# Kernel tuning notes

Hardware: AMD Instinct MI355X
Metric: run time of the kernel (lower is better)

The kernel has to match this reference:

```python
import jax, jax.numpy as jnp
import numpy as np

N_NODES = 100000
N_EDGES = 1600000
F_IN = 128
HIDDEN = 64
N_CLASSES = 32


def setup_inputs() -> dict:
    key = jax.random.key(0)
    k1, k2, k3, k4 = jax.random.split(key, 4)
    x = jax.random.normal(k1, (N_NODES, F_IN), dtype=jnp.float32)
    edge_index = jax.random.randint(k2, (2, N_EDGES), 0, N_NODES, dtype=jnp.int32)
    # Glorot-style init for the two GCNConv weight matrices
    W1 = jax.random.normal(k3, (F_IN, HIDDEN), dtype=jnp.float32) * (1.0 / np.sqrt(F_IN))
    W2 = jax.random.normal(k4, (HIDDEN, N_CLASSES), dtype=jnp.float32) * (1.0 / np.sqrt(HIDDEN))
    b1 = jnp.zeros((HIDDEN,), dtype=jnp.float32)
    b2 = jnp.zeros((N_CLASSES,), dtype=jnp.float32)
    return {"x": x, "edge_index": edge_index, "W1": W1, "b1": b1, "W2": W2, "b2": b2}


def gcn_conv(x, W, b, src, dst, num_nodes):
    # PyG GCNConv: linear transform first, then normalized neighbor aggregation.
    h = x @ W  # [N, out]
    ones = jnp.ones(src.shape, dtype=h.dtype)
    deg = jax.ops.segment_sum(ones, dst, num_segments=num_nodes)  # in-degree incl. self-loops
    d_inv_sqrt = jnp.where(deg > 0, jax.lax.rsqrt(deg), 0.0)
    norm = d_inv_sqrt[src] * d_inv_sqrt[dst]  # [E]
    msg = h[src] * norm[:, None]              # gather + scale, [E, out]
    out = jax.ops.segment_sum(msg, dst, num_segments=num_nodes)  # scatter-add
    return out + b


def reference(x, edge_index, W1, b1, W2, b2):
    n = x.shape[0]
    # add_self_loops=True (GCNConv default)
    loop = jnp.arange(n, dtype=edge_index.dtype)
    src = jnp.concatenate([edge_index[0], loop])
    dst = jnp.concatenate([edge_index[1], loop])
    h = jax.nn.relu(gcn_conv(x, W1, b1, src, dst, n))
    # F.dropout(training=self.training) is identity in eval mode
    logits = gcn_conv(h, W2, b2, src, dst, n)
    return jax.nn.log_softmax(logits, axis=1)
```

## Files before the change

### kernel.cpp

```cpp
#include <hip/hip_runtime.h>

#define F_IN 128
#define HID 64
#define CLS 32
#define BCAP 8192

typedef short v8s __attribute__((ext_vector_type(8)));
typedef float f4 __attribute__((ext_vector_type(4)));
typedef float f2 __attribute__((ext_vector_type(2)));

__device__ __forceinline__ float bflo(unsigned int w) { return __uint_as_float(w << 16); }
__device__ __forceinline__ float bfhi(unsigned int w) { return __uint_as_float(w & 0xFFFF0000u); }
__device__ __forceinline__ unsigned short f2bf(float f) {
    unsigned int u = __float_as_uint(f);
    u += 0x7FFFu + ((u >> 16) & 1u);
    return (unsigned short)(u >> 16);
}
__device__ __forceinline__ unsigned int pack2(float lo, float hi) {
    return (unsigned int)f2bf(lo) | ((unsigned int)f2bf(hi) << 16);
}
__device__ __forceinline__ unsigned int relu2(unsigned int w) {
    unsigned int lo = (w & 0x8000u) ? 0u : (w & 0xFFFFu);
    unsigned int hi = (w & 0x80000000u) ? 0u : (w & 0xFFFF0000u);
    return lo | hi;
}
__device__ __forceinline__ unsigned char f2fp8(float v) {
    return (unsigned char)(__builtin_amdgcn_cvt_pk_fp8_f32(v, v, 0, false) & 0xFF);
}

__global__ __launch_bounds__(512) void k_init(int* __restrict__ bCursor, int nb) {
    int i = threadIdx.x;
    if (i < nb) bCursor[i] = i * BCAP;
}

__global__ __launch_bounds__(256) void k_bscatter(const int* __restrict__ src,
                                                  const int* __restrict__ dst,
                                                  int* __restrict__ bCursor,
                                                  int* __restrict__ bucketed, int E, int nb) {
    __shared__ int h[512];
    __shared__ int chunk[512];
    int tid = threadIdx.x;
    for (int i = tid; i < nb; i += 256) h[i] = 0;
    __syncthreads();

    int e0 = blockIdx.x * 2048;
    int myRec[8], myB[8], myRank[8];
#pragma unroll
    for (int k = 0; k < 8; ++k) {
        int e = e0 + k * 256 + tid;
        if (e < E) {
            int d = dst[e];
            myB[k] = d >> 8;
            myRec[k] = src[e] | ((d & 255) << 17);
            myRank[k] = atomicAdd(&h[myB[k]], 1);
        } else {
            myB[k] = -1;
        }
    }
    __syncthreads();
    for (int i = tid; i < nb; i += 256)
        chunk[i] = h[i] ? atomicAdd(&bCursor[i], h[i]) : 0;
    __syncthreads();
#pragma unroll
    for (int k = 0; k < 8; ++k) {
        if (myB[k] >= 0) bucketed[chunk[myB[k]] + myRank[k]] = myRec[k];
    }
}

__global__ __launch_bounds__(256) void k_csr(const int* __restrict__ bCursor,
                                             const int* __restrict__ bucketed,
                                             int* __restrict__ offs, int* __restrict__ ends,
                                             float* __restrict__ dinv, int* __restrict__ csr,
                                             int n) {
    __shared__ int cnt[256];
    __shared__ int s[256];
    __shared__ int cur[256];
    int b = blockIdx.x;
    int node0 = b << 8;
    int tid = threadIdx.x;
    int node = node0 + tid;
    cnt[tid] = 0;
    __syncthreads();
    int p0 = b * BCAP, p1 = bCursor[b];
    for (int p = p0 + tid; p < p1; p += 256) {
        int rec = bucketed[p];
        atomicAdd(&cnt[rec >> 17], 1);
    }
    __syncthreads();
    int v = cnt[tid];
    s[tid] = v;
    __syncthreads();
    for (int off = 1; off < 256; off <<= 1) {
        int t = (tid >= off) ? s[tid - off] : 0;
        __syncthreads();
        s[tid] += t;
        __syncthreads();
    }
    int myoff = p0 + s[tid] - v;
    cur[tid] = myoff;
    if (node < n) {
        offs[node] = myoff;
        ends[node] = myoff + v;
        dinv[node] = rsqrtf((float)(v + 1));
    }
    __syncthreads();
    for (int p = p0 + tid; p < p1; p += 256) {
        int rec = bucketed[p];
        int pos = atomicAdd(&cur[rec >> 17], 1);
        csr[pos] = rec & 0x1FFFF;
    }
}

__global__ __launch_bounds__(256) void k_gemm1(const float* __restrict__ x,
                                               const float* __restrict__ W,
                                               const float* __restrict__ dinv,
                                               unsigned char* __restrict__ y, int n) {
    __shared__ unsigned short Wt[HID * 136];
    int tid = threadIdx.x;
    for (int i = tid; i < F_IN * HID; i += 256) {
        int k = i >> 6, nn = i & 63;
        Wt[nn * 136 + k] = f2bf(W[i]);
    }
    __syncthreads();

    int lane = tid & 63;
    int quad = lane >> 4, c = lane & 15;
    int nstripes = (n + 31) >> 5;
    int stripe = blockIdx.x * 4 + (tid >> 6);
    if (stripe >= nstripes) return;
    int row0 = stripe << 5;

    f4 acc[2][4] = {};
    union { unsigned int u[4]; v8s v; } au;

#pragma unroll
    for (int ks = 0; ks < 4; ++ks) {
        int k0 = ks * 32 + quad * 8;
        v8s a[2];
#pragma unroll
        for (int mt = 0; mt < 2; ++mt) {
            int row = row0 + mt * 16 + c;
            if (row >= n) row = n - 1;
            const float* xp = x + (size_t)row * F_IN + k0;
            float4 lo = *(const float4*)xp;
            float4 hi = *(const float4*)(xp + 4);
            au.u[0] = pack2(lo.x, lo.y);
            au.u[1] = pack2(lo.z, lo.w);
            au.u[2] = pack2(hi.x, hi.y);
            au.u[3] = pack2(hi.z, hi.w);
            a[mt] = au.v;
        }
#pragma unroll
        for (int nt = 0; nt < 4; ++nt) {
            v8s b = *(const v8s*)&Wt[(nt * 16 + c) * 136 + k0];
            acc[0][nt] = __builtin_amdgcn_mfma_f32_16x16x32_bf16(a[0], b, acc[0][nt], 0, 0, 0);
            acc[1][nt] = __builtin_amdgcn_mfma_f32_16x16x32_bf16(a[1], b, acc[1][nt], 0, 0, 0);
        }
    }

#pragma unroll
    for (int mt = 0; mt < 2; ++mt)
#pragma unroll
        for (int reg = 0; reg < 4; ++reg) {
            int row = row0 + mt * 16 + quad * 4 + reg;
            if (row < n) {
                float dd = dinv[row];
#pragma unroll
                for (int nt = 0; nt < 4; ++nt)
                    y[(size_t)row * HID + nt * 16 + c] = f2fp8(acc[mt][nt][reg] * dd);
            }
        }
}

__global__ __launch_bounds__(256) void k_gemm2(const unsigned short* __restrict__ hb,
                                               const float* __restrict__ W,
                                               const float* __restrict__ dinv,
                                               unsigned short* __restrict__ y, int n) {
    __shared__ unsigned short Wt[CLS * 72];
    int tid = threadIdx.x;
    for (int i = tid; i < HID * CLS; i += 256) {
        int k = i >> 5, nn = i & 31;
        Wt[nn * 72 + k] = f2bf(W[i]);
    }
    __syncthreads();

    int lane = tid & 63;
    int quad = lane >> 4, c = lane & 15;
    int nstripes = (n + 31) >> 5;
    int stripe = blockIdx.x * 4 + (tid >> 6);
    if (stripe >= nstripes) return;
    int row0 = stripe << 5;

    f4 acc[2][2] = {};
    union { unsigned int u[4]; v8s v; } au;

#pragma unroll
    for (int ks = 0; ks < 2; ++ks) {
        int k0 = ks * 32 + quad * 8;
        v8s a[2];
#pragma unroll
        for (int mt = 0; mt < 2; ++mt) {
            int row = row0 + mt * 16 + c;
            if (row >= n) row = n - 1;
            uint4 w = *(const uint4*)(hb + (size_t)row * HID + k0);
            au.u[0] = relu2(w.x);
            au.u[1] = relu2(w.y);
            au.u[2] = relu2(w.z);
            au.u[3] = relu2(w.w);
            a[mt] = au.v;
        }
#pragma unroll
        for (int nt = 0; nt < 2; ++nt) {
            v8s b = *(const v8s*)&Wt[(nt * 16 + c) * 72 + k0];
            acc[0][nt] = __builtin_amdgcn_mfma_f32_16x16x32_bf16(a[0], b, acc[0][nt], 0, 0, 0);
            acc[1][nt] = __builtin_amdgcn_mfma_f32_16x16x32_bf16(a[1], b, acc[1][nt], 0, 0, 0);
        }
    }

#pragma unroll
    for (int mt = 0; mt < 2; ++mt)
#pragma unroll
        for (int reg = 0; reg < 4; ++reg) {
            int row = row0 + mt * 16 + quad * 4 + reg;
            if (row < n) {
                float dd = dinv[row];
#pragma unroll
                for (int nt = 0; nt < 2; ++nt)
                    y[(size_t)row * CLS + nt * 16 + c] = f2bf(acc[mt][nt][reg] * dd);
            }
        }
}

__global__ __launch_bounds__(256) void k_gather64(const int* __restrict__ offs,
                                                  const int* __restrict__ ends,
                                                  const int* __restrict__ csr,
                                                  const float* __restrict__ dinv,
                                                  const unsigned char* __restrict__ xw8,
                                                  const float* __restrict__ b,
                                                  unsigned short* __restrict__ hb, int n) {
    int node = blockIdx.x * 16 + (threadIdx.x >> 4);
    if (node >= n) return;
    int l = threadIdx.x & 15;
    int p0 = offs[node], p1 = ends[node];

    unsigned int sw = *(const unsigned int*)(xw8 + (size_t)node * HID + l * 4);
    float dd = dinv[node];

    f2 A0 = {0.f, 0.f}, A1 = A0, B0 = A0, B1 = A0, C0 = A0, C1 = A0, D0 = A0, D1 = A0;
    int p = p0;
    for (; p + 3 < p1; p += 4) {
        int s0 = csr[p], s1 = csr[p + 1], s2 = csr[p + 2], s3 = csr[p + 3];
        unsigned int w0 = *(const unsigned int*)(xw8 + (size_t)s0 * HID + l * 4);
        unsigned int w1 = *(const unsigned int*)(xw8 + (size_t)s1 * HID + l * 4);
        unsigned int w2 = *(const unsigned int*)(xw8 + (size_t)s2 * HID + l * 4);
        unsigned int w3 = *(const unsigned int*)(xw8 + (size_t)s3 * HID + l * 4);
        A0 += __builtin_amdgcn_cvt_pk_f32_fp8(w0, false);
        A1 += __builtin_amdgcn_cvt_pk_f32_fp8(w0, true);
        B0 += __builtin_amdgcn_cvt_pk_f32_fp8(w1, false);
        B1 += __builtin_amdgcn_cvt_pk_f32_fp8(w1, true);
        C0 += __builtin_amdgcn_cvt_pk_f32_fp8(w2, false);
        C1 += __builtin_amdgcn_cvt_pk_f32_fp8(w2, true);
        D0 += __builtin_amdgcn_cvt_pk_f32_fp8(w3, false);
        D1 += __builtin_amdgcn_cvt_pk_f32_fp8(w3, true);
    }
    for (; p < p1; ++p) {
        int s = csr[p];
        unsigned int w = *(const unsigned int*)(xw8 + (size_t)s * HID + l * 4);
        A0 += __builtin_amdgcn_cvt_pk_f32_fp8(w, false);
        A1 += __builtin_amdgcn_cvt_pk_f32_fp8(w, true);
    }
    A0 += B0; C0 += D0; A0 += C0;
    A1 += B1; C1 += D1; A1 += C1;

    A0 += __builtin_amdgcn_cvt_pk_f32_fp8(sw, false);
    A1 += __builtin_amdgcn_cvt_pk_f32_fp8(sw, true);
    float4 bb = *(const float4*)(b + l * 4);
    uint2 o;
    o.x = pack2(A0.x * dd + bb.x, A0.y * dd + bb.y);
    o.y = pack2(A1.x * dd + bb.z, A1.y * dd + bb.w);
    *(uint2*)(hb + (size_t)node * HID + l * 4) = o;
}

__global__ __launch_bounds__(256) void k_gather32_lsm(const int* __restrict__ offs,
                                                      const int* __restrict__ ends,
                                                      const int* __restrict__ csr,
                                                      const float* __restrict__ dinv,
                                                      const unsigned short* __restrict__ hwb,
                                                      const float* __restrict__ b,
                                                      float* __restrict__ out, int n) {
    int node = blockIdx.x * 16 + (threadIdx.x >> 4);
    if (node >= n) return;
    int l = threadIdx.x & 15;
    int p0 = offs[node], p1 = ends[node];

    unsigned int sw = *(const unsigned int*)(hwb + (size_t)node * CLS + l * 2);
    float dd = dinv[node];

    float A0 = 0.f, A1 = 0.f, B0 = 0.f, B1 = 0.f, C0 = 0.f, C1 = 0.f, D0 = 0.f, D1 = 0.f;
    int p = p0;
    for (; p + 3 < p1; p += 4) {
        int s0 = csr[p], s1 = csr[p + 1], s2 = csr[p + 2], s3 = csr[p + 3];
        unsigned int w0 = *(const unsigned int*)(hwb + (size_t)s0 * CLS + l * 2);
        unsigned int w1 = *(const unsigned int*)(hwb + (size_t)s1 * CLS + l * 2);
        unsigned int w2 = *(const unsigned int*)(hwb + (size_t)s2 * CLS + l * 2);
        unsigned int w3 = *(const unsigned int*)(hwb + (size_t)s3 * CLS + l * 2);
        A0 += bflo(w0); A1 += bfhi(w0);
        B0 += bflo(w1); B1 += bfhi(w1);
        C0 += bflo(w2); C1 += bfhi(w2);
        D0 += bflo(w3); D1 += bfhi(w3);
    }
    for (; p < p1; ++p) {
        int s = csr[p];
        unsigned int w = *(const unsigned int*)(hwb + (size_t)s * CLS + l * 2);
        A0 += bflo(w); A1 += bfhi(w);
    }
    A0 += B0; C0 += D0; A0 += C0;
    A1 += B1; C1 += D1; A1 += C1;

    float v0 = (A0 + bflo(sw)) * dd + b[l * 2];
    float v1 = (A1 + bfhi(sw)) * dd + b[l * 2 + 1];

    float m = fmaxf(v0, v1);
    m = fmaxf(m, __shfl_xor(m, 1));
    m = fmaxf(m, __shfl_xor(m, 2));
    m = fmaxf(m, __shfl_xor(m, 4));
    m = fmaxf(m, __shfl_xor(m, 8));
    float s = __expf(v0 - m) + __expf(v1 - m);
    s += __shfl_xor(s, 1);
    s += __shfl_xor(s, 2);
    s += __shfl_xor(s, 4);
    s += __shfl_xor(s, 8);
    float ls = m + __logf(s);
    float2 o;
    o.x = v0 - ls;
    o.y = v1 - ls;
    *(float2*)(out + (size_t)node * CLS + l * 2) = o;
}

extern "C" void kernel_launch(void* const* d_in, const int* in_sizes, int n_in,
                              void* d_out, int out_size, void* d_ws, size_t ws_size,
                              hipStream_t stream) {
    const float* x  = (const float*)d_in[0];
    const int* edge = (const int*)d_in[1];
    const float* W1 = (const float*)d_in[2];
    const float* b1 = (const float*)d_in[3];
    const float* W2 = (const float*)d_in[4];
    const float* b2 = (const float*)d_in[5];
    float* out = (float*)d_out;

    int N = in_sizes[0] / F_IN;
    int E = in_sizes[1] / 2;
    const int* src = edge;
    const int* dst = edge + E;
    int NB = (N + 255) >> 8;

    float* dinv    = (float*)d_ws;
    int* offs      = (int*)(dinv + N);
    int* ends      = offs + N;
    int* bCursor   = ends + N;
    int* csr       = bCursor + 512;
    int* bucketed  = csr + (size_t)NB * BCAP;
    unsigned char* bufA = (unsigned char*)(bucketed + (size_t)NB * BCAP);
    unsigned short* bufB = (unsigned short*)(bufA + (size_t)N * HID);

    k_init<<<1, 512, 0, stream>>>(bCursor, NB);
    k_bscatter<<<(E + 2047) / 2048, 256, 0, stream>>>(src, dst, bCursor, bucketed, E, NB);
    k_csr<<<NB, 256, 0, stream>>>(bCursor, bucketed, offs, ends, dinv, csr, N);

    int nstripes = (N + 31) >> 5;
    int gemmBlocks = (nstripes + 3) / 4;
    int gatherBlocks = (N + 15) / 16;

    k_gemm1<<<gemmBlocks, 256, 0, stream>>>(x, W1, dinv, bufA, N);
    k_gather64<<<gatherBlocks, 256, 0, stream>>>(offs, ends, csr, dinv, bufA, b1, bufB, N);

    k_gemm2<<<gemmBlocks, 256, 0, stream>>>(bufB, W2, dinv, (unsigned short*)bufA, N);
    k_gather32_lsm<<<gatherBlocks, 256, 0, stream>>>(offs, ends, csr, dinv, (unsigned short*)bufA, b2, out, N);
}
```

Before: 219.5 us.

## Sort nodes by degree per block, pack offset/count, unroll gather by 8

```diff
diff --git a/kernel.cpp b/kernel.cpp
--- a/kernel.cpp
+++ b/kernel.cpp
@@ -69,17 +69,20 @@
 
 __global__ __launch_bounds__(256) void k_csr(const int* __restrict__ bCursor,
                                              const int* __restrict__ bucketed,
-                                             int* __restrict__ offs, int* __restrict__ ends,
+                                             int* __restrict__ pk,
                                              float* __restrict__ dinv, int* __restrict__ csr,
-                                             int n) {
+                                             int* __restrict__ order, int n) {
     __shared__ int cnt[256];
     __shared__ int s[256];
     __shared__ int cur[256];
+    __shared__ int hist[64];
+    __shared__ int hbase[64];
     int b = blockIdx.x;
     int node0 = b << 8;
     int tid = threadIdx.x;
     int node = node0 + tid;
     cnt[tid] = 0;
+    if (tid < 64) hist[tid] = 0;
     __syncthreads();
     int p0 = b * BCAP, p1 = bCursor[b];
     for (int p = p0 + tid; p < p1; p += 256) {
@@ -89,6 +92,8 @@
     __syncthreads();
     int v = cnt[tid];
     s[tid] = v;
+    int dkey = (node < n) ? (v > 63 ? 63 : v) : 0;
+    atomicAdd(&hist[dkey], 1);
     __syncthreads();
     for (int off = 1; off < 256; off <<= 1) {
         int t = (tid >= off) ? s[tid - off] : 0;
@@ -96,18 +101,23 @@
         s[tid] += t;
         __syncthreads();
     }
+    if (tid == 0) {
+        int acc = 0;
+        for (int d = 63; d >= 0; --d) { hbase[d] = acc; acc += hist[d]; }
+    }
     int myoff = p0 + s[tid] - v;
     cur[tid] = myoff;
     if (node < n) {
-        offs[node] = myoff;
-        ends[node] = myoff + v;
+        pk[node] = myoff | (v << 22);
         dinv[node] = rsqrtf((float)(v + 1));
     }
     __syncthreads();
+    int pos = atomicAdd(&hbase[dkey], 1);
+    order[node0 + pos] = node;
     for (int p = p0 + tid; p < p1; p += 256) {
         int rec = bucketed[p];
-        int pos = atomicAdd(&cur[rec >> 17], 1);
-        csr[pos] = rec & 0x1FFFF;
+        int q = atomicAdd(&cur[rec >> 17], 1);
+        csr[q] = rec & 0x1FFFF;
     }
 }
 
@@ -231,29 +241,35 @@
         }
 }
 
-__global__ __launch_bounds__(256) void k_gather64(const int* __restrict__ offs,
-                                                  const int* __restrict__ ends,
+__global__ __launch_bounds__(256) void k_gather64(const int* __restrict__ order,
+                                                  const int* __restrict__ pk,
                                                   const int* __restrict__ csr,
-                                                  const float* __restrict__ dinv,
                                                   const unsigned char* __restrict__ xw8,
                                                   const float* __restrict__ b,
                                                   unsigned short* __restrict__ hb, int n) {
-    int node = blockIdx.x * 16 + (threadIdx.x >> 4);
+    int node = order[blockIdx.x * 16 + (threadIdx.x >> 4)];
     if (node >= n) return;
     int l = threadIdx.x & 15;
-    int p0 = offs[node], p1 = ends[node];
-
+    unsigned int pv = (unsigned int)pk[node];
+    int p0 = pv & 0x3FFFFF;
+    int cntv = pv >> 22;
+    int p1 = p0 + cntv;
+    float dd = rsqrtf((float)(cntv + 1));
     unsigned int sw = *(const unsigned int*)(xw8 + (size_t)node * HID + l * 4);
-    float dd = dinv[node];
 
     f2 A0 = {0.f, 0.f}, A1 = A0, B0 = A0, B1 = A0, C0 = A0, C1 = A0, D0 = A0, D1 = A0;
     int p = p0;
-    for (; p + 3 < p1; p += 4) {
-        int s0 = csr[p], s1 = csr[p + 1], s2 = csr[p + 2], s3 = csr[p + 3];
+    for (; p + 7 < p1; p += 8) {
+        int s0 = csr[p],     s1 = csr[p + 1], s2 = csr[p + 2], s3 = csr[p + 3];
+        int s4 = csr[p + 4], s5 = csr[p + 5], s6 = csr[p + 6], s7 = csr[p + 7];
         unsigned int w0 = *(const unsigned int*)(xw8 + (size_t)s0 * HID + l * 4);
         unsigned int w1 = *(const unsigned int*)(xw8 + (size_t)s1 * HID + l * 4);
         unsigned int w2 = *(const unsigned int*)(xw8 + (size_t)s2 * HID + l * 4);
         unsigned int w3 = *(const unsigned int*)(xw8 + (size_t)s3 * HID + l * 4);
+        unsigned int w4 = *(const unsigned int*)(xw8 + (size_t)s4 * HID + l * 4);
+        unsigned int w5 = *(const unsigned int*)(xw8 + (size_t)s5 * HID + l * 4);
+        unsigned int w6 = *(const unsigned int*)(xw8 + (size_t)s6 * HID + l * 4);
+        unsigned int w7 = *(const unsigned int*)(xw8 + (size_t)s7 * HID + l * 4);
         A0 += __builtin_amdgcn_cvt_pk_f32_fp8(w0, false);
         A1 += __builtin_amdgcn_cvt_pk_f32_fp8(w0, true);
         B0 += __builtin_amdgcn_cvt_pk_f32_fp8(w1, false);
@@ -262,6 +278,14 @@
         C1 += __builtin_amdgcn_cvt_pk_f32_fp8(w2, true);
         D0 += __builtin_amdgcn_cvt_pk_f32_fp8(w3, false);
         D1 += __builtin_amdgcn_cvt_pk_f32_fp8(w3, true);
+        A0 += __builtin_amdgcn_cvt_pk_f32_fp8(w4, false);
+        A1 += __builtin_amdgcn_cvt_pk_f32_fp8(w4, true);
+        B0 += __builtin_amdgcn_cvt_pk_f32_fp8(w5, false);
+        B1 += __builtin_amdgcn_cvt_pk_f32_fp8(w5, true);
+        C0 += __builtin_amdgcn_cvt_pk_f32_fp8(w6, false);
+        C1 += __builtin_amdgcn_cvt_pk_f32_fp8(w6, true);
+        D0 += __builtin_amdgcn_cvt_pk_f32_fp8(w7, false);
+        D1 += __builtin_amdgcn_cvt_pk_f32_fp8(w7, true);
     }
     for (; p < p1; ++p) {
         int s = csr[p];
@@ -281,33 +305,43 @@
     *(uint2*)(hb + (size_t)node * HID + l * 4) = o;
 }
 
-__global__ __launch_bounds__(256) void k_gather32_lsm(const int* __restrict__ offs,
-                                                      const int* __restrict__ ends,
+__global__ __launch_bounds__(256) void k_gather32_lsm(const int* __restrict__ order,
+                                                      const int* __restrict__ pk,
                                                       const int* __restrict__ csr,
-                                                      const float* __restrict__ dinv,
                                                       const unsigned short* __restrict__ hwb,
                                                       const float* __restrict__ b,
                                                       float* __restrict__ out, int n) {
-    int node = blockIdx.x * 16 + (threadIdx.x >> 4);
+    int node = order[blockIdx.x * 16 + (threadIdx.x >> 4)];
     if (node >= n) return;
     int l = threadIdx.x & 15;
-    int p0 = offs[node], p1 = ends[node];
-
+    unsigned int pv = (unsigned int)pk[node];
+    int p0 = pv & 0x3FFFFF;
+    int cntv = pv >> 22;
+    int p1 = p0 + cntv;
+    float dd = rsqrtf((float)(cntv + 1));
     unsigned int sw = *(const unsigned int*)(hwb + (size_t)node * CLS + l * 2);
-    float dd = dinv[node];
 
     float A0 = 0.f, A1 = 0.f, B0 = 0.f, B1 = 0.f, C0 = 0.f, C1 = 0.f, D0 = 0.f, D1 = 0.f;
     int p = p0;
-    for (; p + 3 < p1; p += 4) {
-        int s0 = csr[p], s1 = csr[p + 1], s2 = csr[p + 2], s3 = csr[p + 3];
+    for (; p + 7 < p1; p += 8) {
+        int s0 = csr[p],     s1 = csr[p + 1], s2 = csr[p + 2], s3 = csr[p + 3];
+        int s4 = csr[p + 4], s5 = csr[p + 5], s6 = csr[p + 6], s7 = csr[p + 7];
         unsigned int w0 = *(const unsigned int*)(hwb + (size_t)s0 * CLS + l * 2);
         unsigned int w1 = *(const unsigned int*)(hwb + (size_t)s1 * CLS + l * 2);
         unsigned int w2 = *(const unsigned int*)(hwb + (size_t)s2 * CLS + l * 2);
         unsigned int w3 = *(const unsigned int*)(hwb + (size_t)s3 * CLS + l * 2);
+        unsigned int w4 = *(const unsigned int*)(hwb + (size_t)s4 * CLS + l * 2);
+        unsigned int w5 = *(const unsigned int*)(hwb + (size_t)s5 * CLS + l * 2);
+        unsigned int w6 = *(const unsigned int*)(hwb + (size_t)s6 * CLS + l * 2);
+        unsigned int w7 = *(const unsigned int*)(hwb + (size_t)s7 * CLS + l * 2);
         A0 += bflo(w0); A1 += bfhi(w0);
         B0 += bflo(w1); B1 += bfhi(w1);
         C0 += bflo(w2); C1 += bfhi(w2);
         D0 += bflo(w3); D1 += bfhi(w3);
+        A0 += bflo(w4); A1 += bfhi(w4);
+        B0 += bflo(w5); B1 += bfhi(w5);
+        C0 += bflo(w6); C1 += bfhi(w6);
+        D0 += bflo(w7); D1 += bfhi(w7);
     }
     for (; p < p1; ++p) {
         int s = csr[p];
@@ -355,9 +389,9 @@
     int NB = (N + 255) >> 8;
 
     float* dinv    = (float*)d_ws;
-    int* offs      = (int*)(dinv + N);
-    int* ends      = offs + N;
-    int* bCursor   = ends + N;
+    int* pk        = (int*)(dinv + N);
+    int* order     = pk + N;
+    int* bCursor   = order + (size_t)NB * 256;
     int* csr       = bCursor + 512;
     int* bucketed  = csr + (size_t)NB * BCAP;
     unsigned char* bufA = (unsigned char*)(bucketed + (size_t)NB * BCAP);
@@ -365,15 +399,15 @@
 
     k_init<<<1, 512, 0, stream>>>(bCursor, NB);
     k_bscatter<<<(E + 2047) / 2048, 256, 0, stream>>>(src, dst, bCursor, bucketed, E, NB);
-    k_csr<<<NB, 256, 0, stream>>>(bCursor, bucketed, offs, ends, dinv, csr, N);
+    k_csr<<<NB, 256, 0, stream>>>(bCursor, bucketed, pk, dinv, csr, order, N);
 
     int nstripes = (N + 31) >> 5;
     int gemmBlocks = (nstripes + 3) / 4;
-    int gatherBlocks = (N + 15) / 16;
+    int gatherBlocks = NB * 16;
 
     k_gemm1<<<gemmBlocks, 256, 0, stream>>>(x, W1, dinv, bufA, N);
-    k_gather64<<<gatherBlocks, 256, 0, stream>>>(offs, ends, csr, dinv, bufA, b1, bufB, N);
+    k_gather64<<<gatherBlocks, 256, 0, stream>>>(order, pk, csr, bufA, b1, bufB, N);
 
     k_gemm2<<<gemmBlocks, 256, 0, stream>>>(bufB, W2, dinv, (unsigned short*)bufA, N);
-    k_gather32_lsm<<<gatherBlocks, 256, 0, stream>>>(offs, ends, csr, dinv, (unsigned short*)bufA, b2, out, N);
-}
+    k_gather32_lsm<<<gatherBlocks, 256, 0, stream>>>(order, pk, csr, (unsigned short*)bufA, b2, out, N);
+}
```

Result: slower. 226.8 us (+3.3%).

## Fuse layer-1 aggregation with layer-2 GEMM via shared memory and pack CSR offsets

Applied to the files above, without the earlier changes.

```diff
diff --git a/kernel.cpp b/kernel.cpp
--- a/kernel.cpp
+++ b/kernel.cpp
@@ -18,11 +18,6 @@
 }
 __device__ __forceinline__ unsigned int pack2(float lo, float hi) {
     return (unsigned int)f2bf(lo) | ((unsigned int)f2bf(hi) << 16);
-}
-__device__ __forceinline__ unsigned int relu2(unsigned int w) {
-    unsigned int lo = (w & 0x8000u) ? 0u : (w & 0xFFFFu);
-    unsigned int hi = (w & 0x80000000u) ? 0u : (w & 0xFFFF0000u);
-    return lo | hi;
 }
 __device__ __forceinline__ unsigned char f2fp8(float v) {
     return (unsigned char)(__builtin_amdgcn_cvt_pk_fp8_f32(v, v, 0, false) & 0xFF);
@@ -69,7 +64,7 @@
 
 __global__ __launch_bounds__(256) void k_csr(const int* __restrict__ bCursor,
                                              const int* __restrict__ bucketed,
-                                             int* __restrict__ offs, int* __restrict__ ends,
+                                             int* __restrict__ pk,
                                              float* __restrict__ dinv, int* __restrict__ csr,
                                              int n) {
     __shared__ int cnt[256];
@@ -99,15 +94,14 @@
     int myoff = p0 + s[tid] - v;
     cur[tid] = myoff;
     if (node < n) {
-        offs[node] = myoff;
-        ends[node] = myoff + v;
+        pk[node] = myoff | (v << 22);
         dinv[node] = rsqrtf((float)(v + 1));
     }
     __syncthreads();
     for (int p = p0 + tid; p < p1; p += 256) {
         int rec = bucketed[p];
-        int pos = atomicAdd(&cur[rec >> 17], 1);
-        csr[pos] = rec & 0x1FFFF;
+        int q = atomicAdd(&cur[rec >> 17], 1);
+        csr[q] = rec & 0x1FFFF;
     }
 }
 
@@ -172,48 +166,96 @@
         }
 }
 
-__global__ __launch_bounds__(256) void k_gemm2(const unsigned short* __restrict__ hb,
-                                               const float* __restrict__ W,
-                                               const float* __restrict__ dinv,
-                                               unsigned short* __restrict__ y, int n) {
+__global__ __launch_bounds__(256) void k_gg2(const int* __restrict__ pk,
+                                             const int* __restrict__ csr,
+                                             const unsigned char* __restrict__ xw8,
+                                             const float* __restrict__ b1,
+                                             const float* __restrict__ W2,
+                                             const float* __restrict__ dinv,
+                                             unsigned short* __restrict__ y, int n) {
+    __shared__ unsigned short Ht[128 * 72];
     __shared__ unsigned short Wt[CLS * 72];
     int tid = threadIdx.x;
     for (int i = tid; i < HID * CLS; i += 256) {
         int k = i >> 5, nn = i & 31;
-        Wt[nn * 72 + k] = f2bf(W[i]);
+        Wt[nn * 72 + k] = f2bf(W2[i]);
+    }
+
+    int node0 = blockIdx.x * 128;
+    int g = tid >> 4;
+    int l = tid & 15;
+
+    for (int j = 0; j < 8; ++j) {
+        int local = g * 8 + j;
+        int node = node0 + local;
+        if (node >= n) break;
+        unsigned int pv = (unsigned int)pk[node];
+        int p0 = pv & 0x3FFFFF;
+        int cntv = (int)(pv >> 22);
+        int p1 = p0 + cntv;
+        float dd = rsqrtf((float)(cntv + 1));
+        unsigned int sw = *(const unsigned int*)(xw8 + (size_t)node * HID + l * 4);
+
+        f2 A0 = {0.f, 0.f}, A1 = A0, B0 = A0, B1 = A0, C0 = A0, C1 = A0, D0 = A0, D1 = A0;
+        int p = p0;
+        for (; p + 3 < p1; p += 4) {
+            int s0 = csr[p], s1 = csr[p + 1], s2 = csr[p + 2], s3 = csr[p + 3];
+            unsigned int w0 = *(const unsigned int*)(xw8 + (size_t)s0 * HID + l * 4);
+            unsigned int w1 = *(const unsigned int*)(xw8 + (size_t)s1 * HID + l * 4);
+            unsigned int w2 = *(const unsigned int*)(xw8 + (size_t)s2 * HID + l * 4);
+            unsigned int w3 = *(const unsigned int*)(xw8 + (size_t)s3 * HID + l * 4);
+            A0 += __builtin_amdgcn_cvt_pk_f32_fp8(w0, false);
+            A1 += __builtin_amdgcn_cvt_pk_f32_fp8(w0, true);
+            B0 += __builtin_amdgcn_cvt_pk_f32_fp8(w1, false);
+            B1 += __builtin_amdgcn_cvt_pk_f32_fp8(w1, true);
+            C0 += __builtin_amdgcn_cvt_pk_f32_fp8(w2, false);
+            C1 += __builtin_amdgcn_cvt_pk_f32_fp8(w2, true);
+            D0 += __builtin_amdgcn_cvt_pk_f32_fp8(w3, false);
+            D1 += __builtin_amdgcn_cvt_pk_f32_fp8(w3, true);
+        }
+        for (; p < p1; ++p) {
+            int s = csr[p];
+            unsigned int w = *(const unsigned int*)(xw8 + (size_t)s * HID + l * 4);
+            A0 += __builtin_amdgcn_cvt_pk_f32_fp8(w, false);
+            A1 += __builtin_amdgcn_cvt_pk_f32_fp8(w, true);
+        }
+        A0 += B0; C0 += D0; A0 += C0;
+        A1 += B1; C1 += D1; A1 += C1;
+        A0 += __builtin_amdgcn_cvt_pk_f32_fp8(sw, false);
+        A1 += __builtin_amdgcn_cvt_pk_f32_fp8(sw, true);
+
+        float4 bb = *(const float4*)(b1 + l * 4);
+        float v0 = fmaxf(A0.x * dd + bb.x, 0.f);
+        float v1 = fmaxf(A0.y * dd + bb.y, 0.f);
+        float v2 = fmaxf(A1.x * dd + bb.z, 0.f);
+        float v3 = fmaxf(A1.y * dd + bb.w, 0.f);
+        uint2 o;
+        o.x = pack2(v0, v1);
+        o.y = pack2(v2, v3);
+        *(uint2*)&Ht[local * 72 + l * 4] = o;
     }
     __syncthreads();
 
     int lane = tid & 63;
     int quad = lane >> 4, c = lane & 15;
-    int nstripes = (n + 31) >> 5;
-    int stripe = blockIdx.x * 4 + (tid >> 6);
-    if (stripe >= nstripes) return;
-    int row0 = stripe << 5;
+    int w = tid >> 6;
+    int row0 = w * 32;
 
     f4 acc[2][2] = {};
-    union { unsigned int u[4]; v8s v; } au;
-
 #pragma unroll
     for (int ks = 0; ks < 2; ++ks) {
         int k0 = ks * 32 + quad * 8;
         v8s a[2];
 #pragma unroll
         for (int mt = 0; mt < 2; ++mt) {
-            int row = row0 + mt * 16 + c;
-            if (row >= n) row = n - 1;
-            uint4 w = *(const uint4*)(hb + (size_t)row * HID + k0);
-            au.u[0] = relu2(w.x);
-            au.u[1] = relu2(w.y);
-            au.u[2] = relu2(w.z);
-            au.u[3] = relu2(w.w);
-            a[mt] = au.v;
+            int lrow = row0 + mt * 16 + c;
+            a[mt] = *(const v8s*)&Ht[lrow * 72 + k0];
         }
 #pragma unroll
         for (int nt = 0; nt < 2; ++nt) {
-            v8s b = *(const v8s*)&Wt[(nt * 16 + c) * 72 + k0];
-            acc[0][nt] = __builtin_amdgcn_mfma_f32_16x16x32_bf16(a[0], b, acc[0][nt], 0, 0, 0);
-            acc[1][nt] = __builtin_amdgcn_mfma_f32_16x16x32_bf16(a[1], b, acc[1][nt], 0, 0, 0);
+            v8s bfr = *(const v8s*)&Wt[(nt * 16 + c) * 72 + k0];
+            acc[0][nt] = __builtin_amdgcn_mfma_f32_16x16x32_bf16(a[0], bfr, acc[0][nt], 0, 0, 0);
+            acc[1][nt] = __builtin_amdgcn_mfma_f32_16x16x32_bf16(a[1], bfr, acc[1][nt], 0, 0, 0);
         }
     }
 
@@ -221,80 +263,30 @@
     for (int mt = 0; mt < 2; ++mt)
 #pragma unroll
         for (int reg = 0; reg < 4; ++reg) {
-            int row = row0 + mt * 16 + quad * 4 + reg;
-            if (row < n) {
-                float dd = dinv[row];
+            int node = node0 + row0 + mt * 16 + quad * 4 + reg;
+            if (node < n) {
+                float dd2 = dinv[node];
 #pragma unroll
                 for (int nt = 0; nt < 2; ++nt)
-                    y[(size_t)row * CLS + nt * 16 + c] = f2bf(acc[mt][nt][reg] * dd);
+                    y[(size_t)node * CLS + nt * 16 + c] = f2bf(acc[mt][nt][reg] * dd2);
             }
         }
 }
 
-__global__ __launch_bounds__(256) void k_gather64(const int* __restrict__ offs,
-                                                  const int* __restrict__ ends,
-                                                  const int* __restrict__ csr,
-                                                  const float* __restrict__ dinv,
-                                                  const unsigned char* __restrict__ xw8,
-                                                  const float* __restrict__ b,
-                                                  unsigned short* __restrict__ hb, int n) {
-    int node = blockIdx.x * 16 + (threadIdx.x >> 4);
-    if (node >= n) return;
-    int l = threadIdx.x & 15;
-    int p0 = offs[node], p1 = ends[node];
-
-    unsigned int sw = *(const unsigned int*)(xw8 + (size_t)node * HID + l * 4);
-    float dd = dinv[node];
-
-    f2 A0 = {0.f, 0.f}, A1 = A0, B0 = A0, B1 = A0, C0 = A0, C1 = A0, D0 = A0, D1 = A0;
-    int p = p0;
-    for (; p + 3 < p1; p += 4) {
-        int s0 = csr[p], s1 = csr[p + 1], s2 = csr[p + 2], s3 = csr[p + 3];
-        unsigned int w0 = *(const unsigned int*)(xw8 + (size_t)s0 * HID + l * 4);
-        unsigned int w1 = *(const unsigned int*)(xw8 + (size_t)s1 * HID + l * 4);
-        unsigned int w2 = *(const unsigned int*)(xw8 + (size_t)s2 * HID + l * 4);
-        unsigned int w3 = *(const unsigned int*)(xw8 + (size_t)s3 * HID + l * 4);
-        A0 += __builtin_amdgcn_cvt_pk_f32_fp8(w0, false);
-        A1 += __builtin_amdgcn_cvt_pk_f32_fp8(w0, true);
-        B0 += __builtin_amdgcn_cvt_pk_f32_fp8(w1, false);
-        B1 += __builtin_amdgcn_cvt_pk_f32_fp8(w1, true);
-        C0 += __builtin_amdgcn_cvt_pk_f32_fp8(w2, false);
-        C1 += __builtin_amdgcn_cvt_pk_f32_fp8(w2, true);
-        D0 += __builtin_amdgcn_cvt_pk_f32_fp8(w3, false);
-        D1 += __builtin_amdgcn_cvt_pk_f32_fp8(w3, true);
-    }
-    for (; p < p1; ++p) {
-        int s = csr[p];
-        unsigned int w = *(const unsigned int*)(xw8 + (size_t)s * HID + l * 4);
-        A0 += __builtin_amdgcn_cvt_pk_f32_fp8(w, false);
-        A1 += __builtin_amdgcn_cvt_pk_f32_fp8(w, true);
-    }
-    A0 += B0; C0 += D0; A0 += C0;
-    A1 += B1; C1 += D1; A1 += C1;
-
-    A0 += __builtin_amdgcn_cvt_pk_f32_fp8(sw, false);
-    A1 += __builtin_amdgcn_cvt_pk_f32_fp8(sw, true);
-    float4 bb = *(const float4*)(b + l * 4);
-    uint2 o;
-    o.x = pack2(A0.x * dd + bb.x, A0.y * dd + bb.y);
-    o.y = pack2(A1.x * dd + bb.z, A1.y * dd + bb.w);
-    *(uint2*)(hb + (size_t)node * HID + l * 4) = o;
-}
-
-__global__ __launch_bounds__(256) void k_gather32_lsm(const int* __restrict__ offs,
-                                                      const int* __restrict__ ends,
+__global__ __launch_bounds__(256) void k_gather32_lsm(const int* __restrict__ pk,
                                                       const int* __restrict__ csr,
-                                                      const float* __restrict__ dinv,
                                                       const unsigned short* __restrict__ hwb,
                                                       const float* __restrict__ b,
                                                       float* __restrict__ out, int n) {
     int node = blockIdx.x * 16 + (threadIdx.x >> 4);
     if (node >= n) return;
     int l = threadIdx.x & 15;
-    int p0 = offs[node], p1 = ends[node];
-
+    unsigned int pv = (unsigned int)pk[node];
+    int p0 = pv & 0x3FFFFF;
+    int cntv = (int)(pv >> 22);
+    int p1 = p0 + cntv;
+    float dd = rsqrtf((float)(cntv + 1));
     unsigned int sw = *(const unsigned int*)(hwb + (size_t)node * CLS + l * 2);
-    float dd = dinv[node];
 
     float A0 = 0.f, A1 = 0.f, B0 = 0.f, B1 = 0.f, C0 = 0.f, C1 = 0.f, D0 = 0.f, D1 = 0.f;
     int p = p0;
@@ -355,25 +347,23 @@
     int NB = (N + 255) >> 8;
 
     float* dinv    = (float*)d_ws;
-    int* offs      = (int*)(dinv + N);
-    int* ends      = offs + N;
-    int* bCursor   = ends + N;
+    int* pk        = (int*)(dinv + N);
+    int* bCursor   = pk + N;
     int* csr       = bCursor + 512;
     int* bucketed  = csr + (size_t)NB * BCAP;
     unsigned char* bufA = (unsigned char*)(bucketed + (size_t)NB * BCAP);
-    unsigned short* bufB = (unsigned short*)(bufA + (size_t)N * HID);
+    unsigned short* bufC = (unsigned short*)(bufA + (size_t)N * HID);
 
     k_init<<<1, 512, 0, stream>>>(bCursor, NB);
     k_bscatter<<<(E + 2047) / 2048, 256, 0, stream>>>(src, dst, bCursor, bucketed, E, NB);
-    k_csr<<<NB, 256, 0, stream>>>(bCursor, bucketed, offs, ends, dinv, csr, N);
+    k_csr<<<NB, 256, 0, stream>>>(bCursor, bucketed, pk, dinv, csr, N);
 
     int nstripes = (N + 31) >> 5;
     int gemmBlocks = (nstripes + 3) / 4;
-    int gatherBlocks = (N + 15) / 16;
 
     k_gemm1<<<gemmBlocks, 256, 0, stream>>>(x, W1, dinv, bufA, N);
-    k_gather64<<<gatherBlocks, 256, 0, stream>>>(offs, ends, csr, dinv, bufA, b1, bufB, N);
-
-    k_gemm2<<<gemmBlocks, 256, 0, stream>>>(bufB, W2, dinv, (unsigned short*)bufA, N);
-    k_gather32_lsm<<<gatherBlocks, 256, 0, stream>>>(offs, ends, csr, dinv, (unsigned short*)bufA, b2, out, N);
-}
+
+    k_gg2<<<(N + 127) / 128, 256, 0, stream>>>(pk, csr, bufA, b1, W2, dinv, bufC, N);
+
+    k_gather32_lsm<<<(N + 15) / 16, 256, 0, stream>>>(pk, csr, bufC, b2, out, N);
+}
```

Measured after the change: 232.1 us. 1.06x slower.
